# Kernel optimization log

Measured on AMD Instinct MI355X. Metric: run time of the kernel, lower is better.

The kernel has to match this reference:

```python
import jax, jax.numpy as jnp
import numpy as np

WH, WW = 8, 8          # window height/width
N = WH * WW            # tokens per window = 64
DIM = 256              # channels
H = 8                  # heads
HD = DIM // H          # head dim = 32
NW = 1024              # number of windows per image (256/8)^2
B_ = 4096              # num_windows * batch (batch=4)
EPS = 1e-12            # F.normalize eps


def _rel_pos_index():
    # (2,Wh,Ww) coords -> pairwise relative index into bias table, shape (N, N)
    coords = np.stack(np.meshgrid(np.arange(WH), np.arange(WW), indexing='ij'))
    flat = coords.reshape(2, -1)                      # (2, N)
    rel = flat[:, :, None] - flat[:, None, :]         # (2, N, N)
    rel = rel.transpose(1, 2, 0).astype(np.int64)     # (N, N, 2)
    rel[..., 0] += WH - 1
    rel[..., 1] += WW - 1
    rel[..., 0] *= 2 * WW - 1
    return jnp.asarray(rel.sum(-1))                   # (N, N)

_RPI = _rel_pos_index()


def setup_inputs() -> dict:
    key = jax.random.key(0)
    ks = jax.random.split(key, 12)
    x = jax.random.normal(ks[0], (B_, N, DIM), dtype=jnp.float32)
    c = jax.random.normal(ks[1], (B_, N, DIM), dtype=jnp.float32)
    # 0 / -100 additive shifted-window mask, shape (nW, N, N)
    mask = jnp.where(jax.random.uniform(ks[2], (NW, N, N)) < 0.15, -100.0, 0.0).astype(jnp.float32)
    q_w = jax.random.normal(ks[3], (DIM, DIM), dtype=jnp.float32) * 0.02
    q_b = jnp.zeros((DIM,), jnp.float32)
    kv_w = jax.random.normal(ks[4], (2 * DIM, DIM), dtype=jnp.float32) * 0.02
    kv_b = jnp.zeros((2 * DIM,), jnp.float32)
    logit_scale = jnp.log(10.0) * jnp.ones((H, 1, 1), jnp.float32)
    rpb_table = jax.random.normal(ks[5], ((2 * WH - 1) * (2 * WW - 1), H), dtype=jnp.float32) * 0.02
    proj_w = jax.random.normal(ks[6], (DIM, DIM), dtype=jnp.float32) * 0.02
    proj_b = jnp.zeros((DIM,), jnp.float32)
    return {"x": x, "c": c, "mask": mask, "q_w": q_w, "q_b": q_b,
            "kv_w": kv_w, "kv_b": kv_b, "logit_scale": logit_scale,
            "rpb_table": rpb_table, "proj_w": proj_w, "proj_b": proj_b}


def _l2norm(t):
    n = jnp.sqrt(jnp.sum(t * t, axis=-1, keepdims=True))
    return t / jnp.maximum(n, EPS)


def reference(x, c, mask, q_w, q_b, kv_w, kv_b, logit_scale, rpb_table, proj_w, proj_b):
    Bw, n, Cdim = x.shape
    q = (x @ q_w.T + q_b).reshape(Bw, n, H, HD).transpose(0, 2, 1, 3)      # (B_,H,N,hd)
    kv = (c @ kv_w.T + kv_b).reshape(Bw, n, 2, H, HD).transpose(2, 0, 3, 1, 4)
    k, v = kv[0], kv[1]                                                     # (B_,H,N,hd)
    # cosine-similarity attention with learned clamped logit scale
    attn = jnp.einsum('bhnd,bhmd->bhnm', _l2norm(q), _l2norm(k))
    scale = jnp.exp(jnp.minimum(logit_scale, jnp.log(1.0 / 0.01)))          # (H,1,1)
    attn = attn * scale[None]
    # relative position bias gather: (N,N,H) -> (H,N,N)
    bias = rpb_table[_RPI.reshape(-1)].reshape(n, n, H).transpose(2, 0, 1)
    attn = attn + bias[None]
    # shifted-window mask
    attn = attn.reshape(Bw // NW, NW, H, n, n) + mask[None, :, None]
    attn = jax.nn.softmax(attn.reshape(Bw, H, n, n), axis=-1)
    out = jnp.einsum('bhnm,bhmd->bhnd', attn, v).transpose(0, 2, 1, 3).reshape(Bw, n, Cdim)
    return out @ proj_w.T + proj_b
```

## Files before the change

kernel.cpp:

```cpp
#include <hip/hip_runtime.h>
#include <hip/hip_bf16.h>


typedef __attribute__((ext_vector_type(4))) float f32x4;
typedef __attribute__((ext_vector_type(8))) short bf16x8;
typedef __attribute__((ext_vector_type(4))) unsigned int u32x4;
typedef __attribute__((ext_vector_type(2))) unsigned int u32x2;
typedef __attribute__((ext_vector_type(4))) unsigned short u16x4;

#define MFMA16(a, b, c) __builtin_amdgcn_mfma_f32_16x16x32_bf16((a), (b), (c), 0, 0, 0)

union FragAB {
  bf16x8 v;
  ushort u[8];
  u32x4  q4;
  u32x2  q2[2];
};

__device__ __forceinline__ ushort f2b(float f) {
  union { __hip_bfloat16 h; ushort u; } cv;
  cv.h = __float2bfloat16(f);
  return cv.u;
}

__device__ __forceinline__ float b2f(ushort u) {
  union { float f; unsigned int x; } cv;
  cv.x = ((unsigned)u) << 16;
  return cv.f;
}

__device__ __forceinline__ bf16x8 ldfrag(const ushort* p) {
  FragAB f;
  f.q4 = *(const u32x4*)p;
  return f.v;
}

__device__ __forceinline__ bf16x8 ldfrag8(const ushort* p) {
  FragAB f;
  f.q2[0] = *(const u32x2*)p;
  f.q2[1] = *(const u32x2*)(p + 4);
  return f.v;
}

__device__ __forceinline__ f32x4 fzero() {
  f32x4 z = {0.0f, 0.0f, 0.0f, 0.0f};
  return z;
}

__global__ void prep_kernel(const float* __restrict__ qw, const float* __restrict__ kvw,
                            const float* __restrict__ pw, const float* __restrict__ rpb,
                            const float* __restrict__ lsc,
                            ushort* __restrict__ qwb, ushort* __restrict__ kvwb,
                            ushort* __restrict__ pwb, float* __restrict__ bias2,
                            float* __restrict__ scale) {
  int t = blockIdx.x * blockDim.x + threadIdx.x;
  int stride = gridDim.x * blockDim.x;
  for (int i = t; i < 256 * 256; i += stride) {
    int o = i >> 8, rem = i & 255;
    int kg = rem >> 5, r2 = rem & 31, lg = r2 >> 3, e = r2 & 7;
    int k = (kg << 5) + (lg << 2) + (e < 4 ? e : e + 12);
    qwb[i] = f2b(qw[(o << 8) + k]);
    pwb[i] = f2b(pw[(o << 8) + k]);
  }
  for (int i = t; i < 512 * 256; i += stride) {
    int o = i >> 8, rem = i & 255;
    int kg = rem >> 5, r2 = rem & 31, lg = r2 >> 3, e = r2 & 7;
    int k = (kg << 5) + (lg << 2) + (e < 4 ? e : e + 12);
    kvwb[i] = f2b(kvw[(o << 8) + k]);
  }
  for (int i = t; i < 8 * 64 * 64; i += stride) {
    int h = i >> 12, n = (i >> 6) & 63, m = i & 63;
    int idx = ((n >> 3) - (m >> 3) + 7) * 15 + ((n & 7) - (m & 7) + 7);
    bias2[i] = rpb[idx * 8 + h];
  }
  if (t < 8) scale[t] = __expf(fminf(lsc[t], 4.6051701859880914f));
}

__global__ __launch_bounds__(512, 4)
void wattn_fused(const float* __restrict__ xg, const float* __restrict__ cg,
                 const float* __restrict__ maskg,
                 const float* __restrict__ qb, const float* __restrict__ kvb,
                 const float* __restrict__ pb,
                 const ushort* __restrict__ qwb, const ushort* __restrict__ kvwb,
                 const ushort* __restrict__ pwb,
                 const float* __restrict__ bias2, const float* __restrict__ scaleg,
                 float* __restrict__ outg) {
  __shared__ __align__(16) ushort xs[64][264];
  __shared__ __align__(16) ushort scr[8][2432];
  __shared__ __align__(16) ushort msk[64][68];

  const int b    = blockIdx.x;
  const int wid  = b & 1023;
  const int tid  = threadIdx.x;
  const int w    = tid >> 6;
  const int lane = tid & 63;
  const int lg   = lane >> 4;
  const int lc   = lane & 15;
  const int c0   = w << 5;

  ushort (*myscr)[36] = (ushort(*)[36])&scr[w][0];
  ushort (*vscr)[76]  = (ushort(*)[76])&scr[w][0];

  {
    const float4* src = (const float4*)(xg + (size_t)b * 16384);
#pragma unroll
    for (int it = 0; it < 8; ++it) {
      int i = tid + it * 512;
      float4 v = src[i];
      int row = i >> 6;
      int col = (i & 63) << 2;
      ushort* p = &xs[row][(col & ~31) + (((col & 15) >> 2) << 3) + ((col & 16) ? 4 : 0)];
      p[0] = f2b(v.x); p[1] = f2b(v.y); p[2] = f2b(v.z); p[3] = f2b(v.w);
    }
    const float4* mp4 = (const float4*)(maskg + (size_t)wid * 4096);
#pragma unroll
    for (int it = 0; it < 2; ++it) {
      int i = tid + it * 512;
      float4 v = mp4[i];
      u16x4 pk;
      pk[0] = f2b(v.x); pk[1] = f2b(v.y); pk[2] = f2b(v.z); pk[3] = f2b(v.w);
      *(u16x4*)&msk[i >> 4][(i & 15) << 2] = pk;
    }
  }
  __syncthreads();

  const int cp0 = ((lc >> 2) << 3) + (lc & 3);

  bf16x8 qf[4];
  {
    f32x4 acc[4][2];
#pragma unroll
    for (int mt = 0; mt < 4; ++mt)
#pragma unroll
      for (int nt = 0; nt < 2; ++nt) acc[mt][nt] = fzero();
#pragma unroll
    for (int kg = 0; kg < 8; ++kg) {
      bf16x8 a[4], bb[2];
#pragma unroll
      for (int mt = 0; mt < 4; ++mt)
        a[mt] = ldfrag(&xs[mt * 16 + lc][(kg << 5) + (lg << 3)]);
#pragma unroll
      for (int nt = 0; nt < 2; ++nt)
        bb[nt] = ldfrag(qwb + ((c0 + nt * 16 + lc) << 8) + (kg << 5) + (lg << 3));
#pragma unroll
      for (int mt = 0; mt < 4; ++mt)
#pragma unroll
        for (int nt = 0; nt < 2; ++nt)
          acc[mt][nt] = MFMA16(a[mt], bb[nt], acc[mt][nt]);
    }
    float bias0 = qb[c0 + lc], bias1 = qb[c0 + 16 + lc];
#pragma unroll
    for (int mt = 0; mt < 4; ++mt) {
#pragma unroll
      for (int reg = 0; reg < 4; ++reg) {
        float v0 = acc[mt][0][reg] + bias0;
        float v1 = acc[mt][1][reg] + bias1;
        float ss = v0 * v0 + v1 * v1;
        ss += __shfl_xor(ss, 1);
        ss += __shfl_xor(ss, 2);
        ss += __shfl_xor(ss, 4);
        ss += __shfl_xor(ss, 8);
        float inv = 1.0f / fmaxf(sqrtf(ss), 1e-12f);
        int row = mt * 16 + (lg << 2) + reg;
        myscr[row][cp0]     = f2b(v0 * inv);
        myscr[row][cp0 + 4] = f2b(v1 * inv);
      }
    }
#pragma unroll
    for (int t4 = 0; t4 < 4; ++t4)
      qf[t4] = ldfrag8(&myscr[t4 * 16 + lc][lg << 3]);
  }
  __syncthreads();

  {
    const float4* src = (const float4*)(cg + (size_t)b * 16384);
#pragma unroll
    for (int it = 0; it < 8; ++it) {
      int i = tid + it * 512;
      float4 v = src[i];
      int row = i >> 6;
      int col = (i & 63) << 2;
      ushort* p = &xs[row][(col & ~31) + (((col & 15) >> 2) << 3) + ((col & 16) ? 4 : 0)];
      p[0] = f2b(v.x); p[1] = f2b(v.y); p[2] = f2b(v.z); p[3] = f2b(v.w);
    }
  }
  __syncthreads();

  bf16x8 kf[4];
  {
    f32x4 acc[4][2];
#pragma unroll
    for (int mt = 0; mt < 4; ++mt)
#pragma unroll
      for (int nt = 0; nt < 2; ++nt) acc[mt][nt] = fzero();
#pragma unroll
    for (int kg = 0; kg < 8; ++kg) {
      bf16x8 a[4], bb[2];
#pragma unroll
      for (int mt = 0; mt < 4; ++mt)
        a[mt] = ldfrag(&xs[mt * 16 + lc][(kg << 5) + (lg << 3)]);
#pragma unroll
      for (int nt = 0; nt < 2; ++nt)
        bb[nt] = ldfrag(kvwb + ((c0 + nt * 16 + lc) << 8) + (kg << 5) + (lg << 3));
#pragma unroll
      for (int mt = 0; mt < 4; ++mt)
#pragma unroll
        for (int nt = 0; nt < 2; ++nt)
          acc[mt][nt] = MFMA16(a[mt], bb[nt], acc[mt][nt]);
    }
    float bias0 = kvb[c0 + lc], bias1 = kvb[c0 + 16 + lc];
#pragma unroll
    for (int mt = 0; mt < 4; ++mt) {
#pragma unroll
      for (int reg = 0; reg < 4; ++reg) {
        float v0 = acc[mt][0][reg] + bias0;
        float v1 = acc[mt][1][reg] + bias1;
        float ss = v0 * v0 + v1 * v1;
        ss += __shfl_xor(ss, 1);
        ss += __shfl_xor(ss, 2);
        ss += __shfl_xor(ss, 4);
        ss += __shfl_xor(ss, 8);
        float inv = 1.0f / fmaxf(sqrtf(ss), 1e-12f);
        int row = mt * 16 + (lg << 2) + reg;
        myscr[row][cp0]     = f2b(v0 * inv);
        myscr[row][cp0 + 4] = f2b(v1 * inv);
      }
    }
#pragma unroll
    for (int t4 = 0; t4 < 4; ++t4)
      kf[t4] = ldfrag8(&myscr[t4 * 16 + lc][lg << 3]);
  }

  {
    f32x4 acc[4][2];
#pragma unroll
    for (int mt = 0; mt < 4; ++mt)
#pragma unroll
      for (int nt = 0; nt < 2; ++nt) acc[mt][nt] = fzero();
#pragma unroll
    for (int kg = 0; kg < 8; ++kg) {
      bf16x8 a[4], bb[2];
#pragma unroll
      for (int mt = 0; mt < 4; ++mt)
        a[mt] = ldfrag(&xs[mt * 16 + lc][(kg << 5) + (lg << 3)]);
#pragma unroll
      for (int nt = 0; nt < 2; ++nt)
        bb[nt] = ldfrag(kvwb + ((256 + c0 + nt * 16 + lc) << 8) + (kg << 5) + (lg << 3));
#pragma unroll
      for (int mt = 0; mt < 4; ++mt)
#pragma unroll
        for (int nt = 0; nt < 2; ++nt)
          acc[mt][nt] = MFMA16(a[mt], bb[nt], acc[mt][nt]);
    }
    float bias0 = kvb[256 + c0 + lc], bias1 = kvb[256 + c0 + 16 + lc];
#pragma unroll
    for (int mt = 0; mt < 4; ++mt) {
      int off = ((mt >> 1) << 5) | (lg << 3) | ((mt & 1) << 2);
      u16x4 pk0, pk1;
#pragma unroll
      for (int reg = 0; reg < 4; ++reg) {
        pk0[reg] = f2b(acc[mt][0][reg] + bias0);
        pk1[reg] = f2b(acc[mt][1][reg] + bias1);
      }
      *(u16x4*)&vscr[lc][off]      = pk0;
      *(u16x4*)&vscr[16 + lc][off] = pk1;
    }
  }

  u16x4 ov[2][4];
  {
    const float sc = scaleg[w];
    const float* b2 = bias2 + (w << 12);
    FragAB pfr[2][4];
#pragma unroll
    for (int nt = 0; nt < 4; ++nt) {
      f32x4 st[4];
#pragma unroll
      for (int mt = 0; mt < 4; ++mt)
        st[mt] = MFMA16(kf[mt], qf[nt], fzero());
      const int n = nt * 16 + lc;
      float mx = -3.0e38f;
#pragma unroll
      for (int mt = 0; mt < 4; ++mt) {
        f32x4 bv = *(const f32x4*)(b2 + (n << 6) + mt * 16 + (lg << 2));
        u16x4 mk = *(const u16x4*)&msk[n][mt * 16 + (lg << 2)];
#pragma unroll
        for (int reg = 0; reg < 4; ++reg) {
          float val = st[mt][reg] * sc + bv[reg] + b2f(mk[reg]);
          st[mt][reg] = val;
          mx = fmaxf(mx, val);
        }
      }
      mx = fmaxf(mx, __shfl_xor(mx, 16));
      mx = fmaxf(mx, __shfl_xor(mx, 32));
      float sm = 0.0f;
#pragma unroll
      for (int mt = 0; mt < 4; ++mt)
#pragma unroll
        for (int reg = 0; reg < 4; ++reg) {
          float e = __expf(st[mt][reg] - mx);
          st[mt][reg] = e;
          sm += e;
        }
      sm += __shfl_xor(sm, 16);
      sm += __shfl_xor(sm, 32);
      float inv = 1.0f / sm;
#pragma unroll
      for (int kt = 0; kt < 2; ++kt)
#pragma unroll
        for (int j = 0; j < 4; ++j) {
          pfr[kt][nt].u[j]     = f2b(st[2 * kt][j] * inv);
          pfr[kt][nt].u[4 + j] = f2b(st[2 * kt + 1][j] * inv);
        }
    }
    f32x4 ot[2][4];
#pragma unroll
    for (int dmt = 0; dmt < 2; ++dmt)
#pragma unroll
      for (int nt = 0; nt < 4; ++nt) ot[dmt][nt] = fzero();
#pragma unroll
    for (int kt = 0; kt < 2; ++kt) {
      bf16x8 av[2];
#pragma unroll
      for (int dmt = 0; dmt < 2; ++dmt)
        av[dmt] = ldfrag(&vscr[dmt * 16 + lc][(kt << 5) + (lg << 3)]);
#pragma unroll
      for (int nt = 0; nt < 4; ++nt)
#pragma unroll
        for (int dmt = 0; dmt < 2; ++dmt)
          ot[dmt][nt] = MFMA16(av[dmt], pfr[kt][nt].v, ot[dmt][nt]);
    }
#pragma unroll
    for (int dmt = 0; dmt < 2; ++dmt)
#pragma unroll
      for (int nt = 0; nt < 4; ++nt)
#pragma unroll
        for (int reg = 0; reg < 4; ++reg) ov[dmt][nt][reg] = f2b(ot[dmt][nt][reg]);
  }
  __syncthreads();

#pragma unroll
  for (int nt = 0; nt < 4; ++nt) {
    FragAB o8;
    o8.q2[0] = *(u32x2*)&ov[0][nt];
    o8.q2[1] = *(u32x2*)&ov[1][nt];
    *(u32x4*)&xs[nt * 16 + lc][c0 + (lg << 3)] = o8.q4;
  }
  __syncthreads();

  {
    f32x4 acc[4][2];
#pragma unroll
    for (int mt = 0; mt < 4; ++mt)
#pragma unroll
      for (int nt = 0; nt < 2; ++nt) acc[mt][nt] = fzero();
#pragma unroll
    for (int kg = 0; kg < 8; ++kg) {
      bf16x8 a[4], bb[2];
#pragma unroll
      for (int mt = 0; mt < 4; ++mt)
        a[mt] = ldfrag(&xs[mt * 16 + lc][(kg << 5) + (lg << 3)]);
#pragma unroll
      for (int nt = 0; nt < 2; ++nt)
        bb[nt] = ldfrag(pwb + ((c0 + nt * 16 + lc) << 8) + (kg << 5) + (lg << 3));
#pragma unroll
      for (int mt = 0; mt < 4; ++mt)
#pragma unroll
        for (int nt = 0; nt < 2; ++nt)
          acc[mt][nt] = MFMA16(a[mt], bb[nt], acc[mt][nt]);
    }
    float bias0 = pb[c0 + lc], bias1 = pb[c0 + 16 + lc];
    float* op = outg + (size_t)b * 16384;
#pragma unroll
    for (int mt = 0; mt < 4; ++mt) {
#pragma unroll
      for (int reg = 0; reg < 4; ++reg) {
        int row = mt * 16 + (lg << 2) + reg;
        op[(row << 8) + c0 + lc]      = acc[mt][0][reg] + bias0;
        op[(row << 8) + c0 + 16 + lc] = acc[mt][1][reg] + bias1;
      }
    }
  }
}

extern "C" void kernel_launch(void* const* d_in, const int* in_sizes, int n_in,
                              void* d_out, int out_size, void* d_ws, size_t ws_size,
                              hipStream_t stream) {
  const float* x    = (const float*)d_in[0];
  const float* c    = (const float*)d_in[1];
  const float* mask = (const float*)d_in[2];
  const float* q_w  = (const float*)d_in[3];
  const float* q_b  = (const float*)d_in[4];
  const float* kv_w = (const float*)d_in[5];
  const float* kv_b = (const float*)d_in[6];
  const float* lsc  = (const float*)d_in[7];
  const float* rpb  = (const float*)d_in[8];
  const float* p_w  = (const float*)d_in[9];
  const float* p_b  = (const float*)d_in[10];

  char* ws = (char*)d_ws;
  ushort* qwb   = (ushort*)(ws);
  ushort* kvwb  = (ushort*)(ws + 131072);
  ushort* pwb   = (ushort*)(ws + 131072 + 262144);
  float*  bias2 = (float*)(ws + 524288);
  float*  scale = (float*)(ws + 524288 + 131072);

  prep_kernel<<<64, 256, 0, stream>>>(q_w, kv_w, p_w, rpb, lsc, qwb, kvwb, pwb, bias2, scale);
  wattn_fused<<<4096, 512, 0, stream>>>(x, c, mask, q_b, kv_b, p_b, qwb, kvwb, pwb,
                                        bias2, scale, (float*)d_out);
}
```

Measured before the change: 420.1 us.

## Restructure LDS use: swizzled x/c buffers, register-held V, direct fp32 mask reads

Replaces the padded LDS arrays and per-warp scratch with two XOR-swizzled 64x256 bf16 buffers, so x and c are loaded together up front and one barrier between the q and kv phases goes away. Normalized q/k are kept packed in registers and transposed through a swizzled per-warp slab in the c buffer. V fragments stay in registers instead of going through LDS, and the PV MFMA is fused into the softmax loop. The mask is read as fp32 straight from global memory rather than staged in LDS as bf16. This raises register pressure and global mask traffic in exchange for less LDS traffic, fewer bank conflicts and fewer syncs.

```diff
diff --git a/kernel.cpp b/kernel.cpp
--- a/kernel.cpp
+++ b/kernel.cpp
@@ -23,22 +23,9 @@
   return cv.u;
 }
 
-__device__ __forceinline__ float b2f(ushort u) {
-  union { float f; unsigned int x; } cv;
-  cv.x = ((unsigned)u) << 16;
-  return cv.f;
-}
-
 __device__ __forceinline__ bf16x8 ldfrag(const ushort* p) {
   FragAB f;
   f.q4 = *(const u32x4*)p;
-  return f.v;
-}
-
-__device__ __forceinline__ bf16x8 ldfrag8(const ushort* p) {
-  FragAB f;
-  f.q2[0] = *(const u32x2*)p;
-  f.q2[1] = *(const u32x2*)(p + 4);
   return f.v;
 }
 
@@ -85,9 +72,8 @@
                  const ushort* __restrict__ pwb,
                  const float* __restrict__ bias2, const float* __restrict__ scaleg,
                  float* __restrict__ outg) {
-  __shared__ __align__(16) ushort xs[64][264];
-  __shared__ __align__(16) ushort scr[8][2432];
-  __shared__ __align__(16) ushort msk[64][68];
+  __shared__ __align__(16) ushort xs[64 * 256];
+  __shared__ __align__(16) ushort cs[64 * 256];
 
   const int b    = blockIdx.x;
   const int wid  = b & 1023;
@@ -97,36 +83,39 @@
   const int lg   = lane >> 4;
   const int lc   = lane & 15;
   const int c0   = w << 5;
-
-  ushort (*myscr)[36] = (ushort(*)[36])&scr[w][0];
-  ushort (*vscr)[76]  = (ushort(*)[76])&scr[w][0];
-
-  {
-    const float4* src = (const float4*)(xg + (size_t)b * 16384);
+  const int sw4  = (lc & 7) << 4;
+  const int sw3  = (lc & 7) << 3;
+
+  char* xsb = (char*)xs;
+  char* csb = (char*)cs;
+
+  {
+    const float4* srcx = (const float4*)(xg + (size_t)b * 16384);
+    const float4* srcc = (const float4*)(cg + (size_t)b * 16384);
+    float4 rx[8], rc[8];
+#pragma unroll
+    for (int it = 0; it < 8; ++it) rx[it] = srcx[tid + it * 512];
+#pragma unroll
+    for (int it = 0; it < 8; ++it) rc[it] = srcc[tid + it * 512];
 #pragma unroll
     for (int it = 0; it < 8; ++it) {
       int i = tid + it * 512;
-      float4 v = src[i];
       int row = i >> 6;
-      int col = (i & 63) << 2;
-      ushort* p = &xs[row][(col & ~31) + (((col & 15) >> 2) << 3) + ((col & 16) ? 4 : 0)];
-      p[0] = f2b(v.x); p[1] = f2b(v.y); p[2] = f2b(v.z); p[3] = f2b(v.w);
-    }
-    const float4* mp4 = (const float4*)(maskg + (size_t)wid * 4096);
-#pragma unroll
-    for (int it = 0; it < 2; ++it) {
-      int i = tid + it * 512;
-      float4 v = mp4[i];
-      u16x4 pk;
-      pk[0] = f2b(v.x); pk[1] = f2b(v.y); pk[2] = f2b(v.z); pk[3] = f2b(v.w);
-      *(u16x4*)&msk[i >> 4][(i & 15) << 2] = pk;
+      int colf = (i & 63) << 2;
+      int pcb = 2 * ((colf & ~31) + (((colf & 15) >> 2) << 3) + ((colf & 16) ? 4 : 0));
+      int off = row * 512 + (pcb ^ ((row & 7) << 4));
+      u16x4 p0, p1;
+      p0[0] = f2b(rx[it].x); p0[1] = f2b(rx[it].y); p0[2] = f2b(rx[it].z); p0[3] = f2b(rx[it].w);
+      p1[0] = f2b(rc[it].x); p1[1] = f2b(rc[it].y); p1[2] = f2b(rc[it].z); p1[3] = f2b(rc[it].w);
+      *(u16x4*)(xsb + off) = p0;
+      *(u16x4*)(csb + off) = p1;
     }
   }
   __syncthreads();
 
   const int cp0 = ((lc >> 2) << 3) + (lc & 3);
 
-  bf16x8 qf[4];
+  unsigned int qpk[16], kpk[16];
   {
     f32x4 acc[4][2];
 #pragma unroll
@@ -137,8 +126,10 @@
     for (int kg = 0; kg < 8; ++kg) {
       bf16x8 a[4], bb[2];
 #pragma unroll
-      for (int mt = 0; mt < 4; ++mt)
-        a[mt] = ldfrag(&xs[mt * 16 + lc][(kg << 5) + (lg << 3)]);
+      for (int mt = 0; mt < 4; ++mt) {
+        int row = mt * 16 + lc;
+        a[mt] = ldfrag((const ushort*)(xsb + row * 512 + (((kg << 6) + (lg << 4)) ^ sw4)));
+      }
 #pragma unroll
       for (int nt = 0; nt < 2; ++nt)
         bb[nt] = ldfrag(qwb + ((c0 + nt * 16 + lc) << 8) + (kg << 5) + (lg << 3));
@@ -161,32 +152,11 @@
         ss += __shfl_xor(ss, 4);
         ss += __shfl_xor(ss, 8);
         float inv = 1.0f / fmaxf(sqrtf(ss), 1e-12f);
-        int row = mt * 16 + (lg << 2) + reg;
-        myscr[row][cp0]     = f2b(v0 * inv);
-        myscr[row][cp0 + 4] = f2b(v1 * inv);
-      }
-    }
-#pragma unroll
-    for (int t4 = 0; t4 < 4; ++t4)
-      qf[t4] = ldfrag8(&myscr[t4 * 16 + lc][lg << 3]);
-  }
-  __syncthreads();
-
-  {
-    const float4* src = (const float4*)(cg + (size_t)b * 16384);
-#pragma unroll
-    for (int it = 0; it < 8; ++it) {
-      int i = tid + it * 512;
-      float4 v = src[i];
-      int row = i >> 6;
-      int col = (i & 63) << 2;
-      ushort* p = &xs[row][(col & ~31) + (((col & 15) >> 2) << 3) + ((col & 16) ? 4 : 0)];
-      p[0] = f2b(v.x); p[1] = f2b(v.y); p[2] = f2b(v.z); p[3] = f2b(v.w);
-    }
-  }
-  __syncthreads();
-
-  bf16x8 kf[4];
+        qpk[mt * 4 + reg] = (unsigned int)f2b(v0 * inv) | ((unsigned int)f2b(v1 * inv) << 16);
+      }
+    }
+  }
+
   {
     f32x4 acc[4][2];
 #pragma unroll
@@ -197,8 +167,10 @@
     for (int kg = 0; kg < 8; ++kg) {
       bf16x8 a[4], bb[2];
 #pragma unroll
-      for (int mt = 0; mt < 4; ++mt)
-        a[mt] = ldfrag(&xs[mt * 16 + lc][(kg << 5) + (lg << 3)]);
+      for (int mt = 0; mt < 4; ++mt) {
+        int row = mt * 16 + lc;
+        a[mt] = ldfrag((const ushort*)(csb + row * 512 + (((kg << 6) + (lg << 4)) ^ sw4)));
+      }
 #pragma unroll
       for (int nt = 0; nt < 2; ++nt)
         bb[nt] = ldfrag(kvwb + ((c0 + nt * 16 + lc) << 8) + (kg << 5) + (lg << 3));
@@ -221,16 +193,12 @@
         ss += __shfl_xor(ss, 4);
         ss += __shfl_xor(ss, 8);
         float inv = 1.0f / fmaxf(sqrtf(ss), 1e-12f);
-        int row = mt * 16 + (lg << 2) + reg;
-        myscr[row][cp0]     = f2b(v0 * inv);
-        myscr[row][cp0 + 4] = f2b(v1 * inv);
-      }
-    }
-#pragma unroll
-    for (int t4 = 0; t4 < 4; ++t4)
-      kf[t4] = ldfrag8(&myscr[t4 * 16 + lc][lg << 3]);
-  }
-
+        kpk[mt * 4 + reg] = (unsigned int)f2b(v0 * inv) | ((unsigned int)f2b(v1 * inv) << 16);
+      }
+    }
+  }
+
+  FragAB av[2][2];
   {
     f32x4 acc[4][2];
 #pragma unroll
@@ -241,8 +209,10 @@
     for (int kg = 0; kg < 8; ++kg) {
       bf16x8 a[4], bb[2];
 #pragma unroll
-      for (int mt = 0; mt < 4; ++mt)
-        a[mt] = ldfrag(&xs[mt * 16 + lc][(kg << 5) + (lg << 3)]);
+      for (int mt = 0; mt < 4; ++mt) {
+        int row = mt * 16 + lc;
+        a[mt] = ldfrag((const ushort*)(csb + row * 512 + (((kg << 6) + (lg << 4)) ^ sw4)));
+      }
 #pragma unroll
       for (int nt = 0; nt < 2; ++nt)
         bb[nt] = ldfrag(kvwb + ((256 + c0 + nt * 16 + lc) << 8) + (kg << 5) + (lg << 3));
@@ -254,24 +224,69 @@
     }
     float bias0 = kvb[256 + c0 + lc], bias1 = kvb[256 + c0 + 16 + lc];
 #pragma unroll
-    for (int mt = 0; mt < 4; ++mt) {
-      int off = ((mt >> 1) << 5) | (lg << 3) | ((mt & 1) << 2);
-      u16x4 pk0, pk1;
+    for (int kt = 0; kt < 2; ++kt)
+#pragma unroll
+      for (int j = 0; j < 4; ++j) {
+        av[0][kt].u[j]     = f2b(acc[2 * kt][0][j] + bias0);
+        av[0][kt].u[4 + j] = f2b(acc[2 * kt + 1][0][j] + bias0);
+        av[1][kt].u[j]     = f2b(acc[2 * kt][1][j] + bias1);
+        av[1][kt].u[4 + j] = f2b(acc[2 * kt + 1][1][j] + bias1);
+      }
+  }
+  __syncthreads();
+
+  bf16x8 qf[4], kf[4];
+  {
+    char* slab = csb + (w << 12);
+#pragma unroll
+    for (int mt = 0; mt < 4; ++mt)
 #pragma unroll
       for (int reg = 0; reg < 4; ++reg) {
-        pk0[reg] = f2b(acc[mt][0][reg] + bias0);
-        pk1[reg] = f2b(acc[mt][1][reg] + bias1);
-      }
-      *(u16x4*)&vscr[lc][off]      = pk0;
-      *(u16x4*)&vscr[16 + lc][off] = pk1;
-    }
-  }
-
-  u16x4 ov[2][4];
+        int row = mt * 16 + (lg << 2) + reg;
+        int off = row * 64 + ((2 * cp0) ^ ((row & 7) << 3));
+        unsigned int v = qpk[mt * 4 + reg];
+        *(ushort*)(slab + off)       = (ushort)(v & 0xffff);
+        *(ushort*)(slab + (off ^ 8)) = (ushort)(v >> 16);
+      }
+#pragma unroll
+    for (int t4 = 0; t4 < 4; ++t4) {
+      int row = (t4 << 4) + lc;
+      int off = row * 64 + ((lg << 4) ^ sw3);
+      FragAB f;
+      f.q2[0] = *(const u32x2*)(slab + off);
+      f.q2[1] = *(const u32x2*)(slab + (off ^ 8));
+      qf[t4] = f.v;
+    }
+#pragma unroll
+    for (int mt = 0; mt < 4; ++mt)
+#pragma unroll
+      for (int reg = 0; reg < 4; ++reg) {
+        int row = mt * 16 + (lg << 2) + reg;
+        int off = row * 64 + ((2 * cp0) ^ ((row & 7) << 3));
+        unsigned int v = kpk[mt * 4 + reg];
+        *(ushort*)(slab + off)       = (ushort)(v & 0xffff);
+        *(ushort*)(slab + (off ^ 8)) = (ushort)(v >> 16);
+      }
+#pragma unroll
+    for (int t4 = 0; t4 < 4; ++t4) {
+      int row = (t4 << 4) + lc;
+      int off = row * 64 + ((lg << 4) ^ sw3);
+      FragAB f;
+      f.q2[0] = *(const u32x2*)(slab + off);
+      f.q2[1] = *(const u32x2*)(slab + (off ^ 8));
+      kf[t4] = f.v;
+    }
+  }
+
+  f32x4 ot[2][4];
+#pragma unroll
+  for (int dmt = 0; dmt < 2; ++dmt)
+#pragma unroll
+    for (int nt = 0; nt < 4; ++nt) ot[dmt][nt] = fzero();
   {
     const float sc = scaleg[w];
     const float* b2 = bias2 + (w << 12);
-    FragAB pfr[2][4];
+    const float* mq = maskg + (size_t)wid * 4096;
 #pragma unroll
     for (int nt = 0; nt < 4; ++nt) {
       f32x4 st[4];
@@ -282,11 +297,11 @@
       float mx = -3.0e38f;
 #pragma unroll
       for (int mt = 0; mt < 4; ++mt) {
-        f32x4 bv = *(const f32x4*)(b2 + (n << 6) + mt * 16 + (lg << 2));
-        u16x4 mk = *(const u16x4*)&msk[n][mt * 16 + (lg << 2)];
+        f32x4 bv = *(const f32x4*)(b2 + (n << 6) + (mt << 4) + (lg << 2));
+        f32x4 mk = *(const f32x4*)(mq + (n << 6) + (mt << 4) + (lg << 2));
 #pragma unroll
         for (int reg = 0; reg < 4; ++reg) {
-          float val = st[mt][reg] * sc + bv[reg] + b2f(mk[reg]);
+          float val = st[mt][reg] * sc + bv[reg] + mk[reg];
           st[mt][reg] = val;
           mx = fmaxf(mx, val);
         }
@@ -306,45 +321,30 @@
       sm += __shfl_xor(sm, 32);
       float inv = 1.0f / sm;
 #pragma unroll
-      for (int kt = 0; kt < 2; ++kt)
+      for (int kt = 0; kt < 2; ++kt) {
+        FragAB pfr;
 #pragma unroll
         for (int j = 0; j < 4; ++j) {
-          pfr[kt][nt].u[j]     = f2b(st[2 * kt][j] * inv);
-          pfr[kt][nt].u[4 + j] = f2b(st[2 * kt + 1][j] * inv);
+          pfr.u[j]     = f2b(st[2 * kt][j] * inv);
+          pfr.u[4 + j] = f2b(st[2 * kt + 1][j] * inv);
         }
-    }
-    f32x4 ot[2][4];
-#pragma unroll
-    for (int dmt = 0; dmt < 2; ++dmt)
-#pragma unroll
-      for (int nt = 0; nt < 4; ++nt) ot[dmt][nt] = fzero();
-#pragma unroll
-    for (int kt = 0; kt < 2; ++kt) {
-      bf16x8 av[2];
-#pragma unroll
-      for (int dmt = 0; dmt < 2; ++dmt)
-        av[dmt] = ldfrag(&vscr[dmt * 16 + lc][(kt << 5) + (lg << 3)]);
-#pragma unroll
-      for (int nt = 0; nt < 4; ++nt)
 #pragma unroll
         for (int dmt = 0; dmt < 2; ++dmt)
-          ot[dmt][nt] = MFMA16(av[dmt], pfr[kt][nt].v, ot[dmt][nt]);
-    }
-#pragma unroll
-    for (int dmt = 0; dmt < 2; ++dmt)
-#pragma unroll
-      for (int nt = 0; nt < 4; ++nt)
-#pragma unroll
-        for (int reg = 0; reg < 4; ++reg) ov[dmt][nt][reg] = f2b(ot[dmt][nt][reg]);
-  }
-  __syncthreads();
+          ot[dmt][nt] = MFMA16(av[dmt][kt].v, pfr.v, ot[dmt][nt]);
+      }
+    }
+  }
 
 #pragma unroll
   for (int nt = 0; nt < 4; ++nt) {
+    int row = nt * 16 + lc;
     FragAB o8;
-    o8.q2[0] = *(u32x2*)&ov[0][nt];
-    o8.q2[1] = *(u32x2*)&ov[1][nt];
-    *(u32x4*)&xs[nt * 16 + lc][c0 + (lg << 3)] = o8.q4;
+#pragma unroll
+    for (int j = 0; j < 4; ++j) {
+      o8.u[j]     = f2b(ot[0][nt][j]);
+      o8.u[4 + j] = f2b(ot[1][nt][j]);
+    }
+    *(u32x4*)(xsb + row * 512 + (((w << 6) + (lg << 4)) ^ sw4)) = o8.q4;
   }
   __syncthreads();
 
@@ -358,8 +358,10 @@
     for (int kg = 0; kg < 8; ++kg) {
       bf16x8 a[4], bb[2];
 #pragma unroll
-      for (int mt = 0; mt < 4; ++mt)
-        a[mt] = ldfrag(&xs[mt * 16 + lc][(kg << 5) + (lg << 3)]);
+      for (int mt = 0; mt < 4; ++mt) {
+        int row = mt * 16 + lc;
+        a[mt] = ldfrag((const ushort*)(xsb + row * 512 + (((kg << 6) + (lg << 4)) ^ sw4)));
+      }
 #pragma unroll
       for (int nt = 0; nt < 2; ++nt)
         bb[nt] = ldfrag(pwb + ((c0 + nt * 16 + lc) << 8) + (kg << 5) + (lg << 3));
```

New measurement: 633.5 us. +50.8%, slower.
